# Performance work log

Measured on AMD Instinct MI355X. Metric: run time of the kernel, lower is better.

## Reference

```python
import jax, jax.numpy as jnp
import numpy as np

FLT_BACKWARP = 2.5  # Matching.fltBackwarp for intLevel == 4
NEG_SLOPE = 0.1


def backwarp(ten_input, ten_flow):
    # torch grid_sample(mode='bilinear', padding_mode='zeros', align_corners=True)
    # with grid = base + flow*2/(size-1) is equivalent to sampling at pixel coords
    # (x + u, y + v) with zero padding outside [0, W-1] x [0, H-1].
    B, C, H, W = ten_input.shape
    xs = jnp.arange(W, dtype=ten_input.dtype)
    ys = jnp.arange(H, dtype=ten_input.dtype)
    px = xs[None, None, :] + ten_flow[:, 0]  # [B,H,W]
    py = ys[None, :, None] + ten_flow[:, 1]  # [B,H,W]
    x0 = jnp.floor(px)
    y0 = jnp.floor(py)
    x1 = x0 + 1.0
    y1 = y0 + 1.0
    wx1 = px - x0
    wx0 = 1.0 - wx1
    wy1 = py - y0
    wy0 = 1.0 - wy1

    def gather(ix, iy):
        valid = ((ix >= 0) & (ix <= W - 1) & (iy >= 0) & (iy <= H - 1)).astype(ten_input.dtype)
        ixc = jnp.clip(ix, 0, W - 1).astype(jnp.int32)
        iyc = jnp.clip(iy, 0, H - 1).astype(jnp.int32)
        v = jax.vmap(lambda img, yy, xx: img[:, yy, xx])(ten_input, iyc, ixc)  # [B,C,H,W]
        return v * valid[:, None]

    return (gather(x0, y0) * (wx0 * wy0)[:, None]
            + gather(x1, y0) * (wx1 * wy0)[:, None]
            + gather(x0, y1) * (wx0 * wy1)[:, None]
            + gather(x1, y1) * (wx1 * wy1)[:, None])


def correlation(one, two, stride):
    # FunctionCorrelation: 7x7 displacement window, offsets (-3..3)*stride,
    # zero pad 3*stride, dot over channels / C. Output [B,49,ceil(H/s),ceil(W/s)].
    B, C, H, W = one.shape
    p = 3 * stride
    two_pad = jnp.pad(two, ((0, 0), (0, 0), (p, p), (p, p)))
    one_s = one[:, :, ::stride, ::stride]  # [B,C,Ho,Wo]
    outs = []
    for dj in range(-3, 4):  # channel index k = (dj+3)*7 + (di+3)
        for di in range(-3, 4):
            y0 = p + dj * stride
            x0 = p + di * stride
            shift = two_pad[:, :, y0:y0 + H:stride, x0:x0 + W:stride]
            outs.append(jnp.einsum('bchw,bchw->bhw', one_s, shift))
    return jnp.stack(outs, axis=1) / jnp.asarray(C, one.dtype)


def setup_inputs() -> dict:
    key = jax.random.key(0)
    k1, k2, k3 = jax.random.split(key, 3)
    B, C, H, W = 2, 128, 256, 448
    return {
        'tenOne': jax.random.normal(k1, (B, C, H, W), dtype=jnp.float32),
        'tenTwo': jax.random.normal(k2, (B, C, H, W), dtype=jnp.float32),
        'tenFlow': jax.random.normal(k3, (B, 2, H, W), dtype=jnp.float32),
        'intStride': 1,
    }


def reference(tenOne, tenTwo, tenFlow, intStride):
    warped = backwarp(tenTwo, tenFlow * FLT_BACKWARP)
    corr = correlation(tenOne, warped, int(intStride))
    return jax.nn.leaky_relu(corr, NEG_SLOPE)
```

## Files before the change

kernel.cpp:

```cpp
#include <hip/hip_runtime.h>
#include <hip/hip_bf16.h>

#define BB 2
#define CC 128
#define HH 256
#define WW 448
#define KK 49
#define HWSZ (HH * WW)
#define PW 456

#define WT_BYTES ((size_t)BB * HH * PW * CC * 2)
#define TWT_BYTES ((size_t)BB * HH * WW * CC * 2)
#define WS_NEED (WT_BYTES + TWT_BYTES)

typedef __attribute__((ext_vector_type(8))) short bf16x8;
typedef __attribute__((ext_vector_type(4))) float f32x4;
typedef __attribute__((ext_vector_type(8))) unsigned short u16x8;

static __device__ __forceinline__ short f2bf(float v) {
  __hip_bfloat16 h = __float2bfloat16(v);
  return *reinterpret_cast<short*>(&h);
}
static __device__ __forceinline__ float bf2f(unsigned short u) {
  unsigned int x = ((unsigned int)u) << 16;
  return __uint_as_float(x);
}

typedef const __attribute__((address_space(1))) unsigned int* as1_u32p;
typedef __attribute__((address_space(3))) unsigned int* as3_u32p;
static __device__ __forceinline__ void gload_lds16(const void* g, void* l) {
  __builtin_amdgcn_global_load_lds((as1_u32p)g, (as3_u32p)l, 16, 0, 0);
}

__global__ __launch_bounds__(256) void border_kernel(__hip_bfloat16* wt) {
  int i = blockIdx.x * 256 + threadIdx.x;
  int by = i >> 7;
  int r = i & 127;
  int ps = r >> 4;
  int c16 = r & 15;
  int px = (ps < 4) ? ps : (448 + ps);
  u16x8 z = {0, 0, 0, 0, 0, 0, 0, 0};
  *(u16x8*)((char*)wt + ((size_t)((size_t)by * PW + px) * CC + c16 * 8) * 2) = z;
}

__global__ __launch_bounds__(256) void transpose_kernel(
    const float* __restrict__ two, __hip_bfloat16* __restrict__ two_t) {
  __shared__ float lds[128 * 33];
  int bid = blockIdx.x;
  int b = bid / (HWSZ / 32);
  int tile = bid - b * (HWSZ / 32);
  int P0 = tile * 32;

  const float* src = two + (size_t)b * CC * HWSZ + P0;
  int t = threadIdx.x;
  int bc = t >> 3;
  int f = t & 7;
#pragma unroll
  for (int k = 0; k < 4; ++k) {
    int c = bc + k * 32;
    float4 v = *(const float4*)(src + (size_t)c * HWSZ + f * 4);
    float* d = &lds[c * 33 + f * 4];
    d[0] = v.x; d[1] = v.y; d[2] = v.z; d[3] = v.w;
  }
  __syncthreads();

  int q = t & 7;
  int pl = t >> 3;
  int cs = q * 16;
  u16x8 pk0, pk1;
#pragma unroll
  for (int j = 0; j < 8; ++j)
    pk0[j] = (unsigned short)f2bf(lds[(cs + j) * 33 + pl]);
#pragma unroll
  for (int j = 0; j < 8; ++j)
    pk1[j] = (unsigned short)f2bf(lds[(cs + 8 + j) * 33 + pl]);
  char* dst = (char*)two_t + ((size_t)((size_t)b * HWSZ + P0 + pl) * CC + cs) * 2;
  *(u16x8*)dst = pk0;
  *(u16x8*)(dst + 16) = pk1;
}

__global__ __launch_bounds__(1024) void warp_fast(
    const __hip_bfloat16* __restrict__ two_t, const float* __restrict__ flow,
    __hip_bfloat16* __restrict__ wt) {
  int wg = (blockIdx.x & 7) * 64 + (blockIdx.x >> 3);
  int b = wg >> 8;
  int y = wg & 255;
  int pg = threadIdx.x >> 4;
  int cw = threadIdx.x & 15;

  const char* tb = (const char*)two_t + (size_t)b * HWSZ * (CC * 2);
  char* wb = (char*)wt + ((size_t)(b * HH + y) * PW + 4) * (CC * 2);
  const float* fxp = flow + (size_t)(b * 2 + 0) * HWSZ + y * WW;
  const float* fyp = flow + (size_t)(b * 2 + 1) * HWSZ + y * WW;

#pragma unroll 2
  for (int it = 0; it < 7; ++it) {
    int x = it * 64 + pg;

    float fx = fxp[x] * 2.5f;
    float fy = fyp[x] * 2.5f;
    float px = (float)x + fx;
    float py = (float)y + fy;
    float x0f = floorf(px), y0f = floorf(py);
    int x0 = (int)x0f, y0 = (int)y0f;
    int x1 = x0 + 1, y1 = y0 + 1;
    float wx1 = px - x0f, wx0 = 1.0f - wx1;
    float wy1 = py - y0f, wy0 = 1.0f - wy1;
    bool vx0 = (x0 >= 0) && (x0 < WW);
    bool vx1 = (x1 >= 0) && (x1 < WW);
    bool vy0 = (y0 >= 0) && (y0 < HH);
    bool vy1 = (y1 >= 0) && (y1 < HH);
    float w00 = (vx0 && vy0) ? wx0 * wy0 : 0.0f;
    float w01 = (vx1 && vy0) ? wx1 * wy0 : 0.0f;
    float w10 = (vx0 && vy1) ? wx0 * wy1 : 0.0f;
    float w11 = (vx1 && vy1) ? wx1 * wy1 : 0.0f;
    int cx0 = min(max(x0, 0), WW - 1);
    int cx1 = min(max(x1, 0), WW - 1);
    int cy0 = min(max(y0, 0), HH - 1);
    int cy1 = min(max(y1, 0), HH - 1);

    u16x8 a = *(const u16x8*)(tb + ((size_t)cy0 * WW + cx0) * 256 + cw * 16);
    u16x8 bb_ = *(const u16x8*)(tb + ((size_t)cy0 * WW + cx1) * 256 + cw * 16);
    u16x8 c = *(const u16x8*)(tb + ((size_t)cy1 * WW + cx0) * 256 + cw * 16);
    u16x8 d = *(const u16x8*)(tb + ((size_t)cy1 * WW + cx1) * 256 + cw * 16);

    u16x8 pk;
#pragma unroll
    for (int e = 0; e < 8; ++e) {
      float v = w00 * bf2f((unsigned short)a[e]) +
                w01 * bf2f((unsigned short)bb_[e]) +
                w10 * bf2f((unsigned short)c[e]) +
                w11 * bf2f((unsigned short)d[e]);
      pk[e] = (unsigned short)f2bf(v);
    }
    *(u16x8*)(wb + (size_t)x * 256 + cw * 16) = pk;
  }
}

__global__ __launch_bounds__(256) void warp_fallback(
    const float* __restrict__ two, const float* __restrict__ flow,
    __hip_bfloat16* __restrict__ wt) {
  int idx = blockIdx.x * 256 + threadIdx.x;
  if (idx >= BB * HWSZ) return;
  int x = idx % WW;
  int y = (idx / WW) % HH;
  int b = idx / HWSZ;

  float fx = flow[(b * 2 + 0) * HWSZ + y * WW + x] * 2.5f;
  float fy = flow[(b * 2 + 1) * HWSZ + y * WW + x] * 2.5f;
  float px = (float)x + fx;
  float py = (float)y + fy;
  float x0f = floorf(px), y0f = floorf(py);
  int x0 = (int)x0f, y0 = (int)y0f;
  int x1 = x0 + 1, y1 = y0 + 1;
  float wx1 = px - x0f, wx0 = 1.0f - wx1;
  float wy1 = py - y0f, wy0 = 1.0f - wy1;
  bool vx0 = (x0 >= 0) && (x0 < WW);
  bool vx1 = (x1 >= 0) && (x1 < WW);
  bool vy0 = (y0 >= 0) && (y0 < HH);
  bool vy1 = (y1 >= 0) && (y1 < HH);
  float w00 = (vx0 && vy0) ? wx0 * wy0 : 0.0f;
  float w01 = (vx1 && vy0) ? wx1 * wy0 : 0.0f;
  float w10 = (vx0 && vy1) ? wx0 * wy1 : 0.0f;
  float w11 = (vx1 && vy1) ? wx1 * wy1 : 0.0f;
  int cx0 = min(max(x0, 0), WW - 1);
  int cx1 = min(max(x1, 0), WW - 1);
  int cy0 = min(max(y0, 0), HH - 1);
  int cy1 = min(max(y1, 0), HH - 1);
  int o00 = cy0 * WW + cx0;
  int o01 = cy0 * WW + cx1;
  int o10 = cy1 * WW + cx0;
  int o11 = cy1 * WW + cx1;

  const float* p = two + (size_t)b * CC * HWSZ;
  char* wo = (char*)wt + ((size_t)((size_t)(b * HH + y) * PW) + x + 4) * CC * 2;
#pragma unroll 4
  for (int j = 0; j < 16; ++j) {
    u16x8 pk;
#pragma unroll
    for (int jj = 0; jj < 8; ++jj) {
      int c = j * 8 + jj;
      const float* pc = p + (size_t)c * HWSZ;
      float v = w00 * pc[o00] + w01 * pc[o01] + w10 * pc[o10] + w11 * pc[o11];
      pk[jj] = (unsigned short)f2bf(v);
    }
    *(u16x8*)(wo + j * 16) = pk;
  }
}

#define YTB 8
#define NROWS 14
#define NPOS 22
#define ROWCH (NPOS * 16)
#define CHUNKS (NROWS * ROWCH)

__global__ __launch_bounds__(512, 4) void corr_kernel(
    const float* __restrict__ one, const __hip_bfloat16* __restrict__ wt,
    float* __restrict__ out) {
  __shared__ uint4 ldsb[CHUNKS];

  int bid = blockIdx.x;
  int wg = (bid & 7) * 224 + (bid >> 3);
  int b = wg / 896;
  int rem = wg - b * 896;
  int xt = rem >> 5;
  int yt = rem & 31;
  int ybase = yt * YTB;
  int X0 = xt * 16;
  int tid = threadIdx.x;
  int w = tid >> 6;
  int l = tid & 63;
  int lp = l & 15;
  int lg = l >> 4;
  int y = ybase + w;

  const char* wbase =
      (const char*)wt + (((size_t)(b * HH)) * PW + X0 + 1) * (CC * 2);
  bool interior = (ybase >= 3) && (ybase + NROWS - 3 <= HH);

  if (interior) {
#pragma unroll
    for (int k = 0; k < 10; ++k) {
      int ci = tid + k * 512;
      if (k < 9 || tid < (CHUNKS - 9 * 512)) {
        int row = ci / ROWCH;
        int r2 = ci - row * ROWCH;
        int p = r2 >> 4;
        int cw = r2 & 15;
        int cwS = cw ^ (p & 15);
        int yy = ybase - 3 + row;
        const char* g = wbase + (size_t)yy * (PW * CC * 2) + p * 256 + cwS * 16;
        int wave_ci0 = k * 512 + (tid & ~63);
        gload_lds16(g, (char*)ldsb + (size_t)wave_ci0 * 16);
      }
    }
  } else {
#pragma unroll
    for (int k = 0; k < 10; ++k) {
      int ci = tid + k * 512;
      if (ci < CHUNKS) {
        int row = ci / ROWCH;
        int r2 = ci - row * ROWCH;
        int p = r2 >> 4;
        int cw = r2 & 15;
        int yy = ybase - 3 + row;
        uint4 v = {0, 0, 0, 0};
        if (yy >= 0 && yy < HH)
          v = *(const uint4*)(wbase + (size_t)yy * (PW * CC * 2) + p * 256 +
                              cw * 16);
        *(uint4*)((char*)ldsb + ((ci * 16) ^ ((p & 15) << 4))) = v;
      }
    }
  }

  const float* Abase = one + ((size_t)(b * CC) * HH + y) * WW + X0 + lp;
  bf16x8 afr[4];
#pragma unroll
  for (int t = 0; t < 4; ++t)
#pragma unroll
    for (int j = 0; j < 8; ++j)
      afr[t][j] = f2bf(Abase[(size_t)(t * 32 + lg * 8 + j) * HWSZ]);

  __syncthreads();

  int p1 = (lp + 16 < 21) ? (lp + 16) : 21;
  int cosw0[4], cosw1[4];
#pragma unroll
  for (int t = 0; t < 4; ++t) {
    int co = t * 64 + lg * 16;
    cosw0[t] = co ^ ((lp & 15) << 4);
    cosw1[t] = co ^ ((p1 & 15) << 4);
  }

  f32x4 acc[7][2] = {};
#pragma unroll
  for (int dj = 0; dj < 7; ++dj) {
    int rl = w + dj;
    int b0 = (rl * NPOS + lp) << 8;
    int b1 = (rl * NPOS + p1) << 8;
#pragma unroll
    for (int t = 0; t < 4; ++t) {
      bf16x8 v0 = *(const bf16x8*)((const char*)ldsb + (b0 + cosw0[t]));
      bf16x8 v1 = *(const bf16x8*)((const char*)ldsb + (b1 + cosw1[t]));
      acc[dj][0] = __builtin_amdgcn_mfma_f32_16x16x32_bf16(afr[t], v0,
                                                           acc[dj][0], 0, 0, 0);
      acc[dj][1] = __builtin_amdgcn_mfma_f32_16x16x32_bf16(afr[t], v1,
                                                           acc[dj][1], 0, 0, 0);
    }
  }

  __syncthreads();
  float* sc = (float*)ldsb;
#pragma unroll
  for (int dj = 0; dj < 7; ++dj) {
#pragma unroll
    for (int nt = 0; nt < 2; ++nt) {
      int post = lp + 16 * nt;
#pragma unroll
      for (int r = 0; r < 4; ++r) {
        int xlc = 4 * lg + r;
        int di = post - xlc;
        if (di >= 0 && di <= 6) {
          int k = dj * 7 + di;
          sc[k * 128 + w * 16 + ((xlc + k) & 15)] = acc[dj][nt][r];
        }
      }
    }
  }
  __syncthreads();

  float* ob = out + (size_t)(b * KK) * HWSZ + (size_t)ybase * WW + X0;
#pragma unroll
  for (int i = 0; i < 13; ++i) {
    int e = tid + i * 512;
    if (e < KK * 128) {
      int k = e >> 7;
      int yr = (e >> 4) & 7;
      int px = e & 15;
      float v = sc[k * 128 + yr * 16 + ((px + k) & 15)] * (1.0f / 128.0f);
      v = (v > 0.0f) ? v : 0.1f * v;
      ob[(size_t)k * HWSZ + yr * WW + px] = v;
    }
  }
}

extern "C" void kernel_launch(void* const* d_in, const int* in_sizes, int n_in,
                              void* d_out, int out_size, void* d_ws,
                              size_t ws_size, hipStream_t stream) {
  const float* tenOne = (const float*)d_in[0];
  const float* tenTwo = (const float*)d_in[1];
  const float* tenFlow = (const float*)d_in[2];

  __hip_bfloat16* wt = (__hip_bfloat16*)d_ws;
  border_kernel<<<256, 256, 0, stream>>>(wt);

  if (ws_size >= WS_NEED) {
    __hip_bfloat16* two_t = (__hip_bfloat16*)((char*)d_ws + WT_BYTES);
    transpose_kernel<<<BB * (HWSZ / 32), 256, 0, stream>>>(tenTwo, two_t);
    warp_fast<<<512, 1024, 0, stream>>>(two_t, tenFlow, wt);
  } else {
    int blocks = (BB * HWSZ + 255) / 256;
    warp_fallback<<<blocks, 256, 0, stream>>>(tenTwo, tenFlow, wt);
  }
  corr_kernel<<<1792, 512, 0, stream>>>(tenOne, wt, (float*)d_out);
}
```

Before: 136.4 us.

## Fuse bilinear backwarp into correlation kernel tile load

Removes the separate warp and border-zeroing kernels and the padded warped intermediate buffer. The correlation kernel now computes the bilinear warp on the fly from the channel-last bf16 copy while filling its shared-memory tile. This removes a full write and reread of the warped tensor and two launches. In exchange it recomputes warped pixels in overlapping halos, replaces async global-to-LDS loads with gather loads, and lowers the occupancy hint.

```diff
diff --git a/kernel.cpp b/kernel.cpp
--- a/kernel.cpp
+++ b/kernel.cpp
@@ -7,11 +7,8 @@
 #define WW 448
 #define KK 49
 #define HWSZ (HH * WW)
-#define PW 456
-
-#define WT_BYTES ((size_t)BB * HH * PW * CC * 2)
+
 #define TWT_BYTES ((size_t)BB * HH * WW * CC * 2)
-#define WS_NEED (WT_BYTES + TWT_BYTES)
 
 typedef __attribute__((ext_vector_type(8))) short bf16x8;
 typedef __attribute__((ext_vector_type(4))) float f32x4;
@@ -24,23 +21,6 @@
 static __device__ __forceinline__ float bf2f(unsigned short u) {
   unsigned int x = ((unsigned int)u) << 16;
   return __uint_as_float(x);
-}
-
-typedef const __attribute__((address_space(1))) unsigned int* as1_u32p;
-typedef __attribute__((address_space(3))) unsigned int* as3_u32p;
-static __device__ __forceinline__ void gload_lds16(const void* g, void* l) {
-  __builtin_amdgcn_global_load_lds((as1_u32p)g, (as3_u32p)l, 16, 0, 0);
-}
-
-__global__ __launch_bounds__(256) void border_kernel(__hip_bfloat16* wt) {
-  int i = blockIdx.x * 256 + threadIdx.x;
-  int by = i >> 7;
-  int r = i & 127;
-  int ps = r >> 4;
-  int c16 = r & 15;
-  int px = (ps < 4) ? ps : (448 + ps);
-  u16x8 z = {0, 0, 0, 0, 0, 0, 0, 0};
-  *(u16x8*)((char*)wt + ((size_t)((size_t)by * PW + px) * CC + c16 * 8) * 2) = z;
 }
 
 __global__ __launch_bounds__(256) void transpose_kernel(
@@ -79,124 +59,15 @@
   *(u16x8*)(dst + 16) = pk1;
 }
 
-__global__ __launch_bounds__(1024) void warp_fast(
-    const __hip_bfloat16* __restrict__ two_t, const float* __restrict__ flow,
-    __hip_bfloat16* __restrict__ wt) {
-  int wg = (blockIdx.x & 7) * 64 + (blockIdx.x >> 3);
-  int b = wg >> 8;
-  int y = wg & 255;
-  int pg = threadIdx.x >> 4;
-  int cw = threadIdx.x & 15;
-
-  const char* tb = (const char*)two_t + (size_t)b * HWSZ * (CC * 2);
-  char* wb = (char*)wt + ((size_t)(b * HH + y) * PW + 4) * (CC * 2);
-  const float* fxp = flow + (size_t)(b * 2 + 0) * HWSZ + y * WW;
-  const float* fyp = flow + (size_t)(b * 2 + 1) * HWSZ + y * WW;
-
-#pragma unroll 2
-  for (int it = 0; it < 7; ++it) {
-    int x = it * 64 + pg;
-
-    float fx = fxp[x] * 2.5f;
-    float fy = fyp[x] * 2.5f;
-    float px = (float)x + fx;
-    float py = (float)y + fy;
-    float x0f = floorf(px), y0f = floorf(py);
-    int x0 = (int)x0f, y0 = (int)y0f;
-    int x1 = x0 + 1, y1 = y0 + 1;
-    float wx1 = px - x0f, wx0 = 1.0f - wx1;
-    float wy1 = py - y0f, wy0 = 1.0f - wy1;
-    bool vx0 = (x0 >= 0) && (x0 < WW);
-    bool vx1 = (x1 >= 0) && (x1 < WW);
-    bool vy0 = (y0 >= 0) && (y0 < HH);
-    bool vy1 = (y1 >= 0) && (y1 < HH);
-    float w00 = (vx0 && vy0) ? wx0 * wy0 : 0.0f;
-    float w01 = (vx1 && vy0) ? wx1 * wy0 : 0.0f;
-    float w10 = (vx0 && vy1) ? wx0 * wy1 : 0.0f;
-    float w11 = (vx1 && vy1) ? wx1 * wy1 : 0.0f;
-    int cx0 = min(max(x0, 0), WW - 1);
-    int cx1 = min(max(x1, 0), WW - 1);
-    int cy0 = min(max(y0, 0), HH - 1);
-    int cy1 = min(max(y1, 0), HH - 1);
-
-    u16x8 a = *(const u16x8*)(tb + ((size_t)cy0 * WW + cx0) * 256 + cw * 16);
-    u16x8 bb_ = *(const u16x8*)(tb + ((size_t)cy0 * WW + cx1) * 256 + cw * 16);
-    u16x8 c = *(const u16x8*)(tb + ((size_t)cy1 * WW + cx0) * 256 + cw * 16);
-    u16x8 d = *(const u16x8*)(tb + ((size_t)cy1 * WW + cx1) * 256 + cw * 16);
-
-    u16x8 pk;
-#pragma unroll
-    for (int e = 0; e < 8; ++e) {
-      float v = w00 * bf2f((unsigned short)a[e]) +
-                w01 * bf2f((unsigned short)bb_[e]) +
-                w10 * bf2f((unsigned short)c[e]) +
-                w11 * bf2f((unsigned short)d[e]);
-      pk[e] = (unsigned short)f2bf(v);
-    }
-    *(u16x8*)(wb + (size_t)x * 256 + cw * 16) = pk;
-  }
-}
-
-__global__ __launch_bounds__(256) void warp_fallback(
-    const float* __restrict__ two, const float* __restrict__ flow,
-    __hip_bfloat16* __restrict__ wt) {
-  int idx = blockIdx.x * 256 + threadIdx.x;
-  if (idx >= BB * HWSZ) return;
-  int x = idx % WW;
-  int y = (idx / WW) % HH;
-  int b = idx / HWSZ;
-
-  float fx = flow[(b * 2 + 0) * HWSZ + y * WW + x] * 2.5f;
-  float fy = flow[(b * 2 + 1) * HWSZ + y * WW + x] * 2.5f;
-  float px = (float)x + fx;
-  float py = (float)y + fy;
-  float x0f = floorf(px), y0f = floorf(py);
-  int x0 = (int)x0f, y0 = (int)y0f;
-  int x1 = x0 + 1, y1 = y0 + 1;
-  float wx1 = px - x0f, wx0 = 1.0f - wx1;
-  float wy1 = py - y0f, wy0 = 1.0f - wy1;
-  bool vx0 = (x0 >= 0) && (x0 < WW);
-  bool vx1 = (x1 >= 0) && (x1 < WW);
-  bool vy0 = (y0 >= 0) && (y0 < HH);
-  bool vy1 = (y1 >= 0) && (y1 < HH);
-  float w00 = (vx0 && vy0) ? wx0 * wy0 : 0.0f;
-  float w01 = (vx1 && vy0) ? wx1 * wy0 : 0.0f;
-  float w10 = (vx0 && vy1) ? wx0 * wy1 : 0.0f;
-  float w11 = (vx1 && vy1) ? wx1 * wy1 : 0.0f;
-  int cx0 = min(max(x0, 0), WW - 1);
-  int cx1 = min(max(x1, 0), WW - 1);
-  int cy0 = min(max(y0, 0), HH - 1);
-  int cy1 = min(max(y1, 0), HH - 1);
-  int o00 = cy0 * WW + cx0;
-  int o01 = cy0 * WW + cx1;
-  int o10 = cy1 * WW + cx0;
-  int o11 = cy1 * WW + cx1;
-
-  const float* p = two + (size_t)b * CC * HWSZ;
-  char* wo = (char*)wt + ((size_t)((size_t)(b * HH + y) * PW) + x + 4) * CC * 2;
-#pragma unroll 4
-  for (int j = 0; j < 16; ++j) {
-    u16x8 pk;
-#pragma unroll
-    for (int jj = 0; jj < 8; ++jj) {
-      int c = j * 8 + jj;
-      const float* pc = p + (size_t)c * HWSZ;
-      float v = w00 * pc[o00] + w01 * pc[o01] + w10 * pc[o10] + w11 * pc[o11];
-      pk[jj] = (unsigned short)f2bf(v);
-    }
-    *(u16x8*)(wo + j * 16) = pk;
-  }
-}
-
 #define YTB 8
 #define NROWS 14
 #define NPOS 22
 #define ROWCH (NPOS * 16)
 #define CHUNKS (NROWS * ROWCH)
 
-__global__ __launch_bounds__(512, 4) void corr_kernel(
-    const float* __restrict__ one, const __hip_bfloat16* __restrict__ wt,
-    float* __restrict__ out) {
+__global__ __launch_bounds__(512, 2) void corr_fused(
+    const float* __restrict__ one, const __hip_bfloat16* __restrict__ two_t,
+    const float* __restrict__ flow, float* __restrict__ out) {
   __shared__ uint4 ldsb[CHUNKS];
 
   int bid = blockIdx.x;
@@ -214,42 +85,63 @@
   int lg = l >> 4;
   int y = ybase + w;
 
-  const char* wbase =
-      (const char*)wt + (((size_t)(b * HH)) * PW + X0 + 1) * (CC * 2);
-  bool interior = (ybase >= 3) && (ybase + NROWS - 3 <= HH);
-
-  if (interior) {
-#pragma unroll
-    for (int k = 0; k < 10; ++k) {
-      int ci = tid + k * 512;
-      if (k < 9 || tid < (CHUNKS - 9 * 512)) {
-        int row = ci / ROWCH;
-        int r2 = ci - row * ROWCH;
-        int p = r2 >> 4;
-        int cw = r2 & 15;
-        int cwS = cw ^ (p & 15);
-        int yy = ybase - 3 + row;
-        const char* g = wbase + (size_t)yy * (PW * CC * 2) + p * 256 + cwS * 16;
-        int wave_ci0 = k * 512 + (tid & ~63);
-        gload_lds16(g, (char*)ldsb + (size_t)wave_ci0 * 16);
+  const char* tb = (const char*)two_t + (size_t)b * HWSZ * (CC * 2);
+  const float* fxp = flow + (size_t)(b * 2 + 0) * HWSZ;
+  const float* fyp = flow + (size_t)(b * 2 + 1) * HWSZ;
+
+#pragma unroll
+  for (int k = 0; k < 10; ++k) {
+    int ci = tid + k * 512;
+    if (ci < CHUNKS) {
+      int row = ci / ROWCH;
+      int r2 = ci - row * ROWCH;
+      int p = r2 >> 4;
+      int cw = r2 & 15;
+      int yy = ybase - 3 + row;
+      int x = X0 + p - 3;
+      bool vpix = (yy >= 0) && (yy < HH) && (x >= 0) && (x < WW);
+      int yyc = min(max(yy, 0), HH - 1);
+      int xc = min(max(x, 0), WW - 1);
+      float fx = fxp[yyc * WW + xc] * 2.5f;
+      float fy = fyp[yyc * WW + xc] * 2.5f;
+      float pxf = (float)x + fx;
+      float pyf = (float)yy + fy;
+      float x0f = floorf(pxf), y0f = floorf(pyf);
+      int x0 = (int)x0f, y0 = (int)y0f;
+      int x1 = x0 + 1, y1 = y0 + 1;
+      float wx1 = pxf - x0f, wx0 = 1.0f - wx1;
+      float wy1 = pyf - y0f, wy0 = 1.0f - wy1;
+      float gate = vpix ? 1.0f : 0.0f;
+      wy0 *= gate;
+      wy1 *= gate;
+      bool vx0 = (x0 >= 0) && (x0 < WW);
+      bool vx1 = (x1 >= 0) && (x1 < WW);
+      bool vy0 = (y0 >= 0) && (y0 < HH);
+      bool vy1 = (y1 >= 0) && (y1 < HH);
+      float w00 = (vx0 && vy0) ? wx0 * wy0 : 0.0f;
+      float w01 = (vx1 && vy0) ? wx1 * wy0 : 0.0f;
+      float w10 = (vx0 && vy1) ? wx0 * wy1 : 0.0f;
+      float w11 = (vx1 && vy1) ? wx1 * wy1 : 0.0f;
+      int cx0 = min(max(x0, 0), WW - 1);
+      int cx1 = min(max(x1, 0), WW - 1);
+      int cy0 = min(max(y0, 0), HH - 1);
+      int cy1 = min(max(y1, 0), HH - 1);
+
+      u16x8 ca = *(const u16x8*)(tb + ((size_t)cy0 * WW + cx0) * 256 + cw * 16);
+      u16x8 cb = *(const u16x8*)(tb + ((size_t)cy0 * WW + cx1) * 256 + cw * 16);
+      u16x8 cc = *(const u16x8*)(tb + ((size_t)cy1 * WW + cx0) * 256 + cw * 16);
+      u16x8 cd = *(const u16x8*)(tb + ((size_t)cy1 * WW + cx1) * 256 + cw * 16);
+
+      u16x8 pk;
+#pragma unroll
+      for (int e = 0; e < 8; ++e) {
+        float v = w00 * bf2f((unsigned short)ca[e]) +
+                  w01 * bf2f((unsigned short)cb[e]) +
+                  w10 * bf2f((unsigned short)cc[e]) +
+                  w11 * bf2f((unsigned short)cd[e]);
+        pk[e] = (unsigned short)f2bf(v);
       }
-    }
-  } else {
-#pragma unroll
-    for (int k = 0; k < 10; ++k) {
-      int ci = tid + k * 512;
-      if (ci < CHUNKS) {
-        int row = ci / ROWCH;
-        int r2 = ci - row * ROWCH;
-        int p = r2 >> 4;
-        int cw = r2 & 15;
-        int yy = ybase - 3 + row;
-        uint4 v = {0, 0, 0, 0};
-        if (yy >= 0 && yy < HH)
-          v = *(const uint4*)(wbase + (size_t)yy * (PW * CC * 2) + p * 256 +
-                              cw * 16);
-        *(uint4*)((char*)ldsb + ((ci * 16) ^ ((p & 15) << 4))) = v;
-      }
+      *(u16x8*)((char*)ldsb + ((ci * 16) ^ ((p & 15) << 4))) = pk;
     }
   }
 
@@ -331,16 +223,9 @@
   const float* tenTwo = (const float*)d_in[1];
   const float* tenFlow = (const float*)d_in[2];
 
-  __hip_bfloat16* wt = (__hip_bfloat16*)d_ws;
-  border_kernel<<<256, 256, 0, stream>>>(wt);
-
-  if (ws_size >= WS_NEED) {
-    __hip_bfloat16* two_t = (__hip_bfloat16*)((char*)d_ws + WT_BYTES);
-    transpose_kernel<<<BB * (HWSZ / 32), 256, 0, stream>>>(tenTwo, two_t);
-    warp_fast<<<512, 1024, 0, stream>>>(two_t, tenFlow, wt);
-  } else {
-    int blocks = (BB * HWSZ + 255) / 256;
-    warp_fallback<<<blocks, 256, 0, stream>>>(tenTwo, tenFlow, wt);
-  }
-  corr_kernel<<<1792, 512, 0, stream>>>(tenOne, wt, (float*)d_out);
-}
+  __hip_bfloat16* two_t = (__hip_bfloat16*)d_ws;
+
+  transpose_kernel<<<BB * (HWSZ / 32), 256, 0, stream>>>(tenTwo, two_t);
+  corr_fused<<<1792, 512, 0, stream>>>(tenOne, two_t, tenFlow,
+                                       (float*)d_out);
+}
```

Measured after the change: 114.6 us (median of 2 runs). 1.19x faster.
